# Kernel tuning notes

Measured on AMD Instinct MI355X. Metric: run time of the kernel, lower is better.

The kernel has to match this reference:

```python
import jax, jax.numpy as jnp
import numpy as np

B, T, C = 2, 2048, 1024
H, D, R = 16, 64, 32  # heads, head_dim, compression rank (R < D)


def setup_inputs() -> dict:
    key = jax.random.key(0)
    ks = jax.random.split(key, 8)
    s = 0.02
    return {
        "hidden_states": jax.random.normal(ks[0], (B, T, C), jnp.float32),
        "c_attn_w": jax.random.normal(ks[1], (C, 3 * C), jnp.float32) * s,
        "c_attn_b": jnp.zeros((3 * C,), jnp.float32),
        "c_proj_w": jax.random.normal(ks[2], (C, C), jnp.float32) * s,
        "c_proj_b": jnp.zeros((C,), jnp.float32),
        "wk_c": jax.random.normal(ks[3], (D, R), jnp.float32) * (1.0 / np.sqrt(D)),
        "wk_e": jax.random.normal(ks[4], (R, D), jnp.float32) * (1.0 / np.sqrt(R)),
        "wv_c": jax.random.normal(ks[5], (D, R), jnp.float32) * (1.0 / np.sqrt(D)),
        "wv_e": jax.random.normal(ks[6], (R, D), jnp.float32) * (1.0 / np.sqrt(R)),
    }


def reference(hidden_states, c_attn_w, c_attn_b, c_proj_w, c_proj_b,
              wk_c, wk_e, wv_c, wv_e):
    b, t, c = hidden_states.shape
    # GPT2 Conv1D: x @ W + b, then split into Q, K, V
    qkv = hidden_states @ c_attn_w + c_attn_b  # [B,T,3C]
    q, k, v = jnp.split(qkv, 3, axis=-1)

    def split_heads(x):  # [B,T,C] -> [B,H,T,D]
        return x.reshape(b, t, H, D).transpose(0, 2, 1, 3)

    q = split_heads(q)
    k = split_heads(k)
    v = split_heads(v)

    # Low-rank KV compression then expansion (rank R < D path)
    k_lat = jnp.einsum('bhtd,dr->bhtr', k, wk_c)  # [B,H,T,R]
    v_lat = jnp.einsum('bhtd,dr->bhtr', v, wv_c)
    k_exp = jnp.einsum('bhtr,rd->bhtd', k_lat, wk_e)  # [B,H,T,D]
    v_exp = jnp.einsum('bhtr,rd->bhtd', v_lat, wv_e)

    # Causal SDPA (attention_mask is None and q_len > 1 -> is_causal=True)
    scale = 1.0 / np.sqrt(D).astype(np.float32)
    scores = jnp.einsum('bhqd,bhkd->bhqk', q, k_exp) * scale  # [B,H,T,T]
    causal = jnp.tril(jnp.ones((t, t), dtype=bool))
    scores = jnp.where(causal[None, None], scores, jnp.finfo(scores.dtype).min)
    probs = jax.nn.softmax(scores, axis=-1)
    attn = jnp.einsum('bhqk,bhkd->bhqd', probs, v_exp)  # [B,H,T,D]

    # Merge heads and output projection
    attn = attn.transpose(0, 2, 1, 3).reshape(b, t, c)
    out = attn @ c_proj_w + c_proj_b
    return out
```

## Files before the change

kernel.cpp:

```cpp
#include <hip/hip_runtime.h>
#include <cstddef>

typedef __attribute__((ext_vector_type(8))) __bf16 bf16x8;
typedef __attribute__((ext_vector_type(4))) float f32x4;
typedef unsigned short u16;
typedef unsigned int   u32;

#define SCLF (0.125f * 1.44269504f)

__device__ __forceinline__ u16 f2bf(float f){
  union { float f; u32 u; } v; v.f = f;
  u32 r = v.u + 0x7FFFu + ((v.u >> 16) & 1u);
  return (u16)(r >> 16);
}
__device__ __forceinline__ u32 cvtpk(float lo, float hi){
  u32 r; asm("v_cvt_pk_bf16_f32 %0, %1, %2" : "=v"(r) : "v"(lo), "v"(hi)); return r;
}
__device__ __forceinline__ void gll16(const void* g, void* l){
  __builtin_amdgcn_global_load_lds((__attribute__((address_space(1))) void*)g,
                                   (__attribute__((address_space(3))) void*)l, 16, 0, 0);
}

__global__ __launch_bounds__(256) void prep_fused(const float* __restrict__ x,
      const float* __restrict__ Wa, const float* __restrict__ ba, const float* __restrict__ Wp,
      const float* __restrict__ kc, const float* __restrict__ ke,
      const float* __restrict__ vc, const float* __restrict__ ve,
      u16* __restrict__ Xb, float* __restrict__ b2,
      u16* __restrict__ Wt, u16* __restrict__ W2t){
  __shared__ __align__(16) char PS[28928];
  float* SH = (float*)PS;
  u16* As = (u16*)(PS + 16640);
  u16* Bs = (u16*)(PS + 16640 + 8192);
  const int bid = blockIdx.x, tid = threadIdx.x;

  if (bid < 4096){
    int i = bid*256 + tid;
    float4 v = ((const float4*)x)[i];
    uint2 r; r.x = cvtpk(v.x, v.y); r.y = cvtpk(v.z, v.w);
    ((uint2*)Xb)[i] = r;
    return;
  }
  if (bid < 4099){
    const int part = bid - 4096;
    float* BaL = SH;
    float* W65 = SH + 1024;
    *(float4*)&BaL[tid*4] = *(const float4*)&ba[part*1024 + tid*4];
    {
      const float* msrc = (part==0) ? ke : (part==1) ? kc : vc;
      #pragma unroll
      for (int i=0;i<8;++i){
        int idx = tid + i*256;
        float v = msrc[idx];
        int r, d;
        if (part == 0){ r = idx >> 6; d = idx & 63; }
        else          { d = idx >> 5; r = idx & 31; }
        W65[r*65 + d] = v;
      }
    }
    __syncthreads();
    const float scl = (part==0) ? SCLF : 1.f;
    #pragma unroll
    for (int t=0;t<2;++t){
      int l = tid + t*256;
      int hh = l >> 5, r = l & 31;
      float acc = 0.f;
      for (int d=0;d<64;++d) acc += BaL[hh*64 + d] * W65[r*65 + d];
      b2[part*512 + l] = acc * scl;
    }
    return;
  }

  const int wv = tid>>6, ln = tid&63;
  const int lr = ln&15, g8 = (ln>>4)*8, gq = ln>>4;
  const int swz = (lr&7)*8;

  if (bid < 4867){
    const int f = bid - 4099;
    const int cc = f & 15, ph = f >> 4;
    const int part = ph >> 4;
    const int c0 = cc*64;
    {
      int r = tid>>3, d8 = tid&7;
      float v[8];
      if (part == 0){
        #pragma unroll
        for (int j=0;j<8;++j) v[j] = ke[r*64 + d8*8 + j]*SCLF;
      } else {
        const float* m = (part==1) ? kc : vc;
        #pragma unroll
        for (int j=0;j<8;++j) v[j] = m[(d8*8+j)*32 + r];
      }
      uint4 w; w.x=cvtpk(v[0],v[1]); w.y=cvtpk(v[2],v[3]); w.z=cvtpk(v[4],v[5]); w.w=cvtpk(v[6],v[7]);
      *(uint4*)&Bs[r*64 + ((d8 ^ (r&7))*8)] = w;
    }
    #pragma unroll
    for (int p=0;p<2;++p){
      int g2 = p*256 + tid;
      int row = g2>>3, gcol = g2&7;
      const float* src = Wa + (size_t)(c0+row)*3072 + ph*64 + gcol*8;
      float4 a = ((const float4*)src)[0], b = ((const float4*)src)[1];
      uint4 w; w.x=cvtpk(a.x,a.y); w.y=cvtpk(a.z,a.w); w.z=cvtpk(b.x,b.y); w.w=cvtpk(b.z,b.w);
      *(uint4*)&As[row*64 + ((gcol ^ (row&7))*8)] = w;
    }
    __syncthreads();
    f32x4 acc[2] = {};
    const int wr = (wv>>1)*32, wn = wv&1;
    #pragma unroll
    for (int ks=0;ks<2;++ks){
      int off = (ks*32 + g8) ^ swz;
      bf16x8 bf = *(const bf16x8*)&Bs[(wn*16+lr)*64 + off];
      #pragma unroll
      for (int mt=0;mt<2;++mt){
        bf16x8 af = *(const bf16x8*)&As[(wr+mt*16+lr)*64 + off];
        acc[mt] = __builtin_amdgcn_mfma_f32_16x16x32_bf16(af, bf, acc[mt], 0,0,0);
      }
    }
    const int n = part*512 + (ph&15)*32 + wn*16 + lr;
    #pragma unroll
    for (int mt=0;mt<2;++mt){
      union { u16 s[4]; uint2 v; } pk;
      #pragma unroll
      for (int r=0;r<4;++r) pk.s[r] = f2bf(acc[mt][r]);
      *(uint2*)&Wt[(size_t)n*1024 + c0 + wr + mt*16 + 4*gq] = pk.v;
    }
  } else {
    const int f = bid - 4867;
    const int cc = f & 15, ph = f >> 4;
    const int c0 = cc*64;
    {
      int r = tid>>2, c4 = (tid&3)*16;
      const float* src = Wp + (size_t)(ph*64 + r)*1024 + c0 + c4;
      float4 v0 = ((const float4*)src)[0], v1 = ((const float4*)src)[1],
             v2 = ((const float4*)src)[2], v3 = ((const float4*)src)[3];
      float* dst = &SH[r*65 + c4];
      dst[0]=v0.x; dst[1]=v0.y; dst[2]=v0.z; dst[3]=v0.w;
      dst[4]=v1.x; dst[5]=v1.y; dst[6]=v1.z; dst[7]=v1.w;
      dst[8]=v2.x; dst[9]=v2.y; dst[10]=v2.z; dst[11]=v2.w;
      dst[12]=v3.x; dst[13]=v3.y; dst[14]=v3.z; dst[15]=v3.w;
    }
    {
      int r = tid>>3, d8 = tid&7;
      float v[8];
      #pragma unroll
      for (int j=0;j<8;++j) v[j] = ve[r*64 + d8*8 + j];
      uint4 w; w.x=cvtpk(v[0],v[1]); w.y=cvtpk(v[2],v[3]); w.z=cvtpk(v[4],v[5]); w.w=cvtpk(v[6],v[7]);
      *(uint4*)&Bs[r*64 + ((d8 ^ (r&7))*8)] = w;
    }
    __syncthreads();
    #pragma unroll
    for (int p=0;p<2;++p){
      int g2 = p*256 + tid;
      int j = g2>>3, d8 = g2&7;
      float v[8];
      #pragma unroll
      for (int jj=0;jj<8;++jj) v[jj] = SH[(d8*8+jj)*65 + j];
      uint4 w; w.x=cvtpk(v[0],v[1]); w.y=cvtpk(v[2],v[3]); w.z=cvtpk(v[4],v[5]); w.w=cvtpk(v[6],v[7]);
      *(uint4*)&As[j*64 + ((d8 ^ (j&7))*8)] = w;
    }
    __syncthreads();
    f32x4 acc[2] = {};
    const int wr = (wv>>1)*32, wn = wv&1;
    #pragma unroll
    for (int ks=0;ks<2;++ks){
      int off = (ks*32 + g8) ^ swz;
      bf16x8 bf = *(const bf16x8*)&Bs[(wn*16+lr)*64 + off];
      #pragma unroll
      for (int mt=0;mt<2;++mt){
        bf16x8 af = *(const bf16x8*)&As[(wr+mt*16+lr)*64 + off];
        acc[mt] = __builtin_amdgcn_mfma_f32_16x16x32_bf16(af, bf, acc[mt], 0,0,0);
      }
    }
    const int col = ph*32 + wn*16 + lr;
    #pragma unroll
    for (int mt=0;mt<2;++mt)
      #pragma unroll
      for (int r=0;r<4;++r)
        W2t[(size_t)(c0 + wr + mt*16 + 4*gq + r)*512 + col] = f2bf(acc[mt][r]);
  }
}

template<typename OT>
__global__ __launch_bounds__(256) void gemm64(const u16* __restrict__ A, const u16* __restrict__ Bt,
        const float* __restrict__ bias, OT* __restrict__ C, u16* __restrict__ Vt,
        int M, int N, int K, int ldc){
  __shared__ u16 Bs[128*64];
  const int nwg = gridDim.x * gridDim.y;
  const int id  = blockIdx.x + gridDim.x * blockIdx.y;
  const int nid = (id & 7) * (nwg >> 3) + (id >> 3);
  const int bx = nid % gridDim.x, by = nid / gridDim.x;
  const int tid = threadIdx.x, wv = tid>>6, ln = tid&63;
  const int lr = ln&15, g8 = (ln>>4)*8, gq = ln>>4;
  const int m0 = bx*64, n0 = by*128;
  const int wr = (wv>>1)*32, wc = (wv&1)*64;
  const int lrow = ln>>3, lcol = ((ln&7) ^ lrow)*8;
  const int swz = (lr&7)*8;
  const u16* aptr = A + (size_t)(m0 + wr + lr)*K + gq*8;
  f32x4 acc[2][4] = {};
  const int nk = K >> 6;
  for (int kt=0; kt<nk; ++kt){
    #pragma unroll
    for (int it=0; it<4; ++it){
      int bc = wv*4 + it;
      int row = bc*8 + lrow;
      gll16(Bt + (size_t)(n0+row)*K + kt*64 + lcol, &Bs[bc*512]);
    }
    bf16x8 aF[2][2];
    #pragma unroll
    for (int mt=0;mt<2;++mt)
      #pragma unroll
      for (int ks=0;ks<2;++ks)
        aF[mt][ks] = *(const bf16x8*)(aptr + (size_t)(mt*16)*K + kt*64 + ks*32);
    __syncthreads();
    #pragma unroll
    for (int ks=0; ks<2; ++ks){
      int off = (ks*32 + g8) ^ swz;
      bf16x8 bfr[4];
      #pragma unroll
      for (int nt=0;nt<4;++nt) bfr[nt] = *(const bf16x8*)&Bs[(wc+nt*16+lr)*64 + off];
      #pragma unroll
      for (int mt=0;mt<2;++mt)
        #pragma unroll
        for (int nt=0;nt<4;++nt)
          acc[mt][nt] = __builtin_amdgcn_mfma_f32_16x16x32_bf16(aF[mt][ks], bfr[nt], acc[mt][nt], 0,0,0);
    }
    __syncthreads();
  }
  if (Vt && n0 >= 1024){
    #pragma unroll
    for (int mt=0;mt<2;++mt){
      int row0 = m0 + wr + mt*16 + 4*(ln>>4);
      int tin  = row0 & 2047;
      int p0 = 4*((tin>>4)&1) + 8*((tin>>2)&3) + 32*(tin>>5);
      size_t vbase = (size_t)(row0 >> 11) * 512;
      #pragma unroll
      for (int nt=0;nt<4;++nt){
        int col = n0 + wc + nt*16 + lr;
        float bv = bias[col];
        int nlat = col - 1024;
        union { u16 s[4]; uint2 v; } pk;
        #pragma unroll
        for (int r=0;r<4;++r) pk.s[r] = f2bf(acc[mt][nt][r] + bv);
        *(uint2*)&Vt[(vbase + nlat)*2048 + p0] = pk.v;
      }
    }
  } else {
    #pragma unroll
    for (int mt=0;mt<2;++mt){
      int row = m0 + wr + mt*16 + 4*(ln>>4);
      #pragma unroll
      for (int nt=0;nt<4;++nt){
        int col = n0 + wc + nt*16 + lr;
        float bv = bias[col];
        #pragma unroll
        for (int r=0;r<4;++r){
          float v = acc[mt][nt][r] + bv;
          if constexpr (sizeof(OT) == 2) C[(size_t)(row+r)*ldc + col] = f2bf(v);
          else                           C[(size_t)(row+r)*ldc + col] = v;
        }
      }
    }
  }
}

__global__ __launch_bounds__(256, 4) void attn_fwd(const u16* __restrict__ QKV,
            const u16* __restrict__ Vt, u16* __restrict__ Out){
  const int bh = blockIdx.x;
  const int y = blockIdx.y;
  const int qt = (y < 8) ? y : (y < 16) ? 23 - y : (y < 24) ? y : 55 - y;
  const int b = bh >> 4, h = bh & 15;
  const int tid = threadIdx.x, wv = tid>>6, ln = tid&63;
  const int sg = wv>>1, wvL = wv&1;
  const int lr = ln&15, gq = ln>>4;
  __shared__ __align__(16) char SMEM[32768];
  u16* KB0 = (u16*)SMEM           + (sg*2    )*2048;
  u16* KB1 = (u16*)SMEM           + (sg*2 + 1)*2048;
  u16* VB0 = (u16*)(SMEM + 16384) + (sg*2    )*2048;
  u16* VB1 = (u16*)(SMEM + 16384) + (sg*2 + 1)*2048;
  const int q0 = qt*64;
  const size_t base = (size_t)(b*2048) * 1536;
  const u16* qrowA = QKV + base + (size_t)(q0 + wvL*32 + lr)*1536 + h*32;
  bf16x8 qfA = *(const bf16x8*)(qrowA + gq*8);
  bf16x8 qfB = *(const bf16x8*)(qrowA + (size_t)16*1536 + gq*8);
  const int qgA = q0 + wvL*32 + lr, qgB = qgA + 16;
  f32x4 oA0 = {}, oA1 = {}, oB0 = {}, oB1 = {};
  float lA = 0.f, lB = 0.f;
  const u16* ksrc = QKV + base + 512 + h*32;
  const u16* vsrc = Vt + (size_t)(bh*32)*2048;

  const int ci = wvL*64 + ln;
  const int rK = ci>>2, cK = 8*((ci&3) ^ (rK&3));
  const int rV = ci>>3, cV = 8*((ci&7) ^ (rV&7));

  int offK[4], offV[2][2];
  #pragma unroll
  for (int nt=0;nt<4;++nt)
    offK[nt] = (nt*16+lr)*64 + ((gq*16) ^ ((lr&3)<<4));
  #pragma unroll
  for (int dt=0;dt<2;++dt)
    #pragma unroll
    for (int c=0;c<2;++c)
      offV[dt][c] = (dt*16+lr)*128 + ((c*64 + gq*16) ^ ((lr&7)<<4));

  if (sg <= qt){
    gll16(ksrc + (size_t)(sg*64 + rK)*1536 + cK,      KB0 + wvL*512);
    gll16(ksrc + (size_t)(sg*64 + 32 + rK)*1536 + cK, KB0 + 1024 + wvL*512);
    gll16(vsrc + (size_t)rV*2048 + sg*64 + cV,        VB0 + wvL*512);
    gll16(vsrc + (size_t)(16+rV)*2048 + sg*64 + cV,   VB0 + 1024 + wvL*512);
  }
  __syncthreads();
  const u16* kpa = ksrc + (size_t)(sg*64 + 128 + rK)*1536 + cK;
  const u16* kpb = ksrc + (size_t)(sg*64 + 160 + rK)*1536 + cK;
  const u16* vpa = vsrc + (size_t)rV*2048 + sg*64 + 128 + cV;
  const u16* vpb = vsrc + (size_t)(16+rV)*2048 + sg*64 + 128 + cV;
  const size_t KSTEP = (size_t)128*1536;

  #define ABODY(II, KBC, VBC, KBN, VBN) do { \
    const int kt = 2*(II) + sg; \
    if (kt + 2 <= qt){ \
      gll16(kpa, (KBN) + wvL*512); \
      gll16(kpb, (KBN) + 1024 + wvL*512); \
      gll16(vpa, (VBN) + wvL*512); \
      gll16(vpb, (VBN) + 1024 + wvL*512); \
      kpa += KSTEP; kpb += KSTEP; vpa += 128; vpb += 128; \
    } \
    if (kt <= qt){ \
      f32x4 sA[4] = {}, sB[4] = {}; \
      __builtin_amdgcn_s_setprio(1); \
      _Pragma("unroll") for (int nt=0;nt<4;++nt){ \
        bf16x8 k0 = *(const bf16x8*)((const char*)(KBC) + offK[nt]); \
        sA[nt] = __builtin_amdgcn_mfma_f32_16x16x32_bf16(k0, qfA, sA[nt], 0,0,0); \
        sB[nt] = __builtin_amdgcn_mfma_f32_16x16x32_bf16(k0, qfB, sB[nt], 0,0,0); \
      } \
      __builtin_amdgcn_s_setprio(0); \
      if (kt == qt){ \
        const int kv0 = kt*64; \
        _Pragma("unroll") for (int nt=0;nt<4;++nt) \
        _Pragma("unroll") for (int r=0;r<4;++r){ \
          int k = kv0 + nt*16 + 4*gq + r; \
          if (k > qgA) sA[nt][r] = -1e30f; \
          if (k > qgB) sB[nt][r] = -1e30f; \
        } \
      } \
      union { u32 u[4]; bf16x8 v; } paA0, paA1, paB0, paB1; \
      { \
        float p0,p1,p2,p3,p4,p5,p6,p7; \
        p0=__builtin_amdgcn_exp2f(sA[0][0]); p1=__builtin_amdgcn_exp2f(sA[0][1]); \
        p2=__builtin_amdgcn_exp2f(sA[0][2]); p3=__builtin_amdgcn_exp2f(sA[0][3]); \
        p4=__builtin_amdgcn_exp2f(sA[1][0]); p5=__builtin_amdgcn_exp2f(sA[1][1]); \
        p6=__builtin_amdgcn_exp2f(sA[1][2]); p7=__builtin_amdgcn_exp2f(sA[1][3]); \
        lA += ((p0+p1)+(p2+p3)) + ((p4+p5)+(p6+p7)); \
        paA0.u[0]=cvtpk(p0,p1); paA0.u[1]=cvtpk(p2,p3); paA0.u[2]=cvtpk(p4,p5); paA0.u[3]=cvtpk(p6,p7); \
        p0=__builtin_amdgcn_exp2f(sA[2][0]); p1=__builtin_amdgcn_exp2f(sA[2][1]); \
        p2=__builtin_amdgcn_exp2f(sA[2][2]); p3=__builtin_amdgcn_exp2f(sA[2][3]); \
        p4=__builtin_amdgcn_exp2f(sA[3][0]); p5=__builtin_amdgcn_exp2f(sA[3][1]); \
        p6=__builtin_amdgcn_exp2f(sA[3][2]); p7=__builtin_amdgcn_exp2f(sA[3][3]); \
        lA += ((p0+p1)+(p2+p3)) + ((p4+p5)+(p6+p7)); \
        paA1.u[0]=cvtpk(p0,p1); paA1.u[1]=cvtpk(p2,p3); paA1.u[2]=cvtpk(p4,p5); paA1.u[3]=cvtpk(p6,p7); \
        p0=__builtin_amdgcn_exp2f(sB[0][0]); p1=__builtin_amdgcn_exp2f(sB[0][1]); \
        p2=__builtin_amdgcn_exp2f(sB[0][2]); p3=__builtin_amdgcn_exp2f(sB[0][3]); \
        p4=__builtin_amdgcn_exp2f(sB[1][0]); p5=__builtin_amdgcn_exp2f(sB[1][1]); \
        p6=__builtin_amdgcn_exp2f(sB[1][2]); p7=__builtin_amdgcn_exp2f(sB[1][3]); \
        lB += ((p0+p1)+(p2+p3)) + ((p4+p5)+(p6+p7)); \
        paB0.u[0]=cvtpk(p0,p1); paB0.u[1]=cvtpk(p2,p3); paB0.u[2]=cvtpk(p4,p5); paB0.u[3]=cvtpk(p6,p7); \
        p0=__builtin_amdgcn_exp2f(sB[2][0]); p1=__builtin_amdgcn_exp2f(sB[2][1]); \
        p2=__builtin_amdgcn_exp2f(sB[2][2]); p3=__builtin_amdgcn_exp2f(sB[2][3]); \
        p4=__builtin_amdgcn_exp2f(sB[3][0]); p5=__builtin_amdgcn_exp2f(sB[3][1]); \
        p6=__builtin_amdgcn_exp2f(sB[3][2]); p7=__builtin_amdgcn_exp2f(sB[3][3]); \
        lB += ((p0+p1)+(p2+p3)) + ((p4+p5)+(p6+p7)); \
        paB1.u[0]=cvtpk(p0,p1); paB1.u[1]=cvtpk(p2,p3); paB1.u[2]=cvtpk(p4,p5); paB1.u[3]=cvtpk(p6,p7); \
      } \
      __builtin_amdgcn_s_setprio(1); \
      { \
        bf16x8 v00 = *(const bf16x8*)((const char*)(VBC) + offV[0][0]); \
        bf16x8 v10 = *(const bf16x8*)((const char*)(VBC) + offV[1][0]); \
        bf16x8 v01 = *(const bf16x8*)((const char*)(VBC) + offV[0][1]); \
        bf16x8 v11 = *(const bf16x8*)((const char*)(VBC) + offV[1][1]); \
        oA0 = __builtin_amdgcn_mfma_f32_16x16x32_bf16(paA0.v, v00, oA0, 0,0,0); \
        oA1 = __builtin_amdgcn_mfma_f32_16x16x32_bf16(paA0.v, v10, oA1, 0,0,0); \
        oB0 = __builtin_amdgcn_mfma_f32_16x16x32_bf16(paB0.v, v00, oB0, 0,0,0); \
        oB1 = __builtin_amdgcn_mfma_f32_16x16x32_bf16(paB0.v, v10, oB1, 0,0,0); \
        oA0 = __builtin_amdgcn_mfma_f32_16x16x32_bf16(paA1.v, v01, oA0, 0,0,0); \
        oA1 = __builtin_amdgcn_mfma_f32_16x16x32_bf16(paA1.v, v11, oA1, 0,0,0); \
        oB0 = __builtin_amdgcn_mfma_f32_16x16x32_bf16(paB1.v, v01, oB0, 0,0,0); \
        oB1 = __builtin_amdgcn_mfma_f32_16x16x32_bf16(paB1.v, v11, oB1, 0,0,0); \
      } \
      __builtin_amdgcn_s_setprio(0); \
    } \
    __syncthreads(); \
  } while(0)

  const int nmax = (qt + 2) >> 1;
  const int jmax = (nmax + 1) >> 1;
  for (int j = 0; j < jmax; ++j){
    ABODY(2*j,   KB0, VB0, KB1, VB1);
    ABODY(2*j+1, KB1, VB1, KB0, VB0);
  }
  lA += __shfl_xor(lA, 16); lA += __shfl_xor(lA, 32);
  lB += __shfl_xor(lB, 16); lB += __shfl_xor(lB, 32);

  float* MO = (float*)SMEM;
  float* ML = (float*)(SMEM + 12288);
  if (sg == 1){
    #pragma unroll
    for (int r=0;r<4;++r){
      int rowA = wvL*32 + 4*gq + r;
      MO[rowA*34 + lr]            = oA0[r];
      MO[rowA*34 + 16 + lr]       = oA1[r];
      MO[(rowA+16)*34 + lr]       = oB0[r];
      MO[(rowA+16)*34 + 16 + lr]  = oB1[r];
    }
    if (gq == 0){ ML[wvL*32 + lr] = lA; ML[wvL*32 + 16 + lr] = lB; }
  }
  __syncthreads();
  if (sg == 0){
    float lSA = lA + ML[wvL*32 + lr];
    float lSB = lB + ML[wvL*32 + 16 + lr];
    float lA_o[4], lB_o[4];
    #pragma unroll
    for (int r=0;r<4;++r){ lA_o[r] = __shfl(lSA, 4*gq + r); lB_o[r] = __shfl(lSB, 4*gq + r); }
    #pragma unroll
    for (int r=0;r<4;++r){
      int rowA = wvL*32 + 4*gq + r;
      float vA0 = (oA0[r] + MO[rowA*34 + lr])           / lA_o[r];
      float vA1 = (oA1[r] + MO[rowA*34 + 16 + lr])      / lA_o[r];
      float vB0 = (oB0[r] + MO[(rowA+16)*34 + lr])      / lB_o[r];
      float vB1 = (oB1[r] + MO[(rowA+16)*34 + 16 + lr]) / lB_o[r];
      size_t obA = (size_t)(b*2048 + q0 + rowA)*512 + h*32;
      Out[obA + lr]      = f2bf(vA0);
      Out[obA + 16 + lr] = f2bf(vA1);
      size_t obB = obA + (size_t)16*512;
      Out[obB + lr]      = f2bf(vB0);
      Out[obB + 16 + lr] = f2bf(vB1);
    }
  }
}

#define WS_B2   0u
#define WS_WT   8192u
#define WS_W2T  (WS_WT + 3145728u)
#define WS_XB   (WS_W2T + 1048576u)
#define WS_QKV  (WS_XB + 8388608u)
#define WS_VT   (WS_QKV + 12582912u)
#define WS_ATT  (WS_VT + 4194304u)

extern "C" void kernel_launch(void* const* d_in, const int* in_sizes, int n_in,
                              void* d_out, int out_size, void* d_ws, size_t ws_size,
                              hipStream_t stream) {
  const float* x  = (const float*)d_in[0];
  const float* Wa = (const float*)d_in[1];
  const float* ba = (const float*)d_in[2];
  const float* Wp = (const float*)d_in[3];
  const float* bp = (const float*)d_in[4];
  const float* kc = (const float*)d_in[5];
  const float* ke = (const float*)d_in[6];
  const float* vc = (const float*)d_in[7];
  const float* ve = (const float*)d_in[8];
  float* out = (float*)d_out;
  char* ws = (char*)d_ws;
  float* b2  = (float*)(ws + WS_B2);
  u16* Wt    = (u16*)(ws + WS_WT);
  u16* W2t   = (u16*)(ws + WS_W2T);
  u16* Xb    = (u16*)(ws + WS_XB);
  u16* QKVb  = (u16*)(ws + WS_QKV);
  u16* Vt    = (u16*)(ws + WS_VT);
  u16* Att   = (u16*)(ws + WS_ATT);

  prep_fused<<<5123, 256, 0, stream>>>(x, Wa, ba, Wp, kc, ke, vc, ve, Xb, b2, Wt, W2t);
  gemm64<u16><<<dim3(64,12), 256, 0, stream>>>(Xb, Wt, b2, QKVb, Vt, 4096, 1536, 1024, 1536);
  attn_fwd<<<dim3(32,32), 256, 0, stream>>>(QKVb, Vt, Att);
  gemm64<float><<<dim3(64,8), 256, 0, stream>>>(Att, W2t, bp, out, (u16*)nullptr, 4096, 1024, 512, 1024);
}
```

Before: 83.01 us.

## Split prep kernel and stage GEMM A tiles through LDS via async loads

Splits the monolithic prep kernel into an x-conversion/bias kernel that handles four float4 elements per thread, and a separate weight-folding kernel launched on a 2D grid. In gemm64 the A operand now goes into LDS with global_load_lds, using the same swizzle as B, instead of being read directly from global memory into registers. This is meant to give coalesced A loads and fewer scattered global reads, at the cost of more LDS, one extra kernel launch, and LDS reads for the A fragments.

```diff
diff --git a/kernel.cpp b/kernel.cpp
--- a/kernel.cpp
+++ b/kernel.cpp
@@ -21,27 +21,23 @@
                                    (__attribute__((address_space(3))) void*)l, 16, 0, 0);
 }
 
-__global__ __launch_bounds__(256) void prep_fused(const float* __restrict__ x,
-      const float* __restrict__ Wa, const float* __restrict__ ba, const float* __restrict__ Wp,
-      const float* __restrict__ kc, const float* __restrict__ ke,
-      const float* __restrict__ vc, const float* __restrict__ ve,
-      u16* __restrict__ Xb, float* __restrict__ b2,
-      u16* __restrict__ Wt, u16* __restrict__ W2t){
-  __shared__ __align__(16) char PS[28928];
-  float* SH = (float*)PS;
-  u16* As = (u16*)(PS + 16640);
-  u16* Bs = (u16*)(PS + 16640 + 8192);
+__global__ __launch_bounds__(256) void prep_x(const float* __restrict__ x,
+      const float* __restrict__ ba, const float* __restrict__ kc,
+      const float* __restrict__ ke, const float* __restrict__ vc,
+      u16* __restrict__ Xb, float* __restrict__ b2){
+  __shared__ float SH[3104];
   const int bid = blockIdx.x, tid = threadIdx.x;
-
-  if (bid < 4096){
-    int i = bid*256 + tid;
-    float4 v = ((const float4*)x)[i];
-    uint2 r; r.x = cvtpk(v.x, v.y); r.y = cvtpk(v.z, v.w);
-    ((uint2*)Xb)[i] = r;
-    return;
-  }
-  if (bid < 4099){
-    const int part = bid - 4096;
+  if (bid < 1024){
+    int i0 = bid*1024 + tid;
+    #pragma unroll
+    for (int t=0;t<4;++t){
+      int i = i0 + t*256;
+      float4 v = ((const float4*)x)[i];
+      uint2 r; r.x = cvtpk(v.x, v.y); r.y = cvtpk(v.z, v.w);
+      ((uint2*)Xb)[i] = r;
+    }
+  } else {
+    const int part = bid - 1024;
     float* BaL = SH;
     float* W65 = SH + 1024;
     *(float4*)&BaL[tid*4] = *(const float4*)&ba[part*1024 + tid*4];
@@ -67,18 +63,27 @@
       for (int d=0;d<64;++d) acc += BaL[hh*64 + d] * W65[r*65 + d];
       b2[part*512 + l] = acc * scl;
     }
-    return;
-  }
-
+  }
+}
+
+__global__ __launch_bounds__(256) void fold_f32(const float* __restrict__ Wa,
+      const float* __restrict__ Wp, const float* __restrict__ kc,
+      const float* __restrict__ ke, const float* __restrict__ vc,
+      const float* __restrict__ ve, u16* __restrict__ Wt, u16* __restrict__ W2t){
+  __shared__ __align__(16) char PS[28928];
+  float* SH = (float*)PS;
+  u16* As = (u16*)(PS + 16640);
+  u16* Bs = (u16*)(PS + 16640 + 8192);
+  const int cc = blockIdx.x, y = blockIdx.y;
+  const int tid = threadIdx.x;
   const int wv = tid>>6, ln = tid&63;
   const int lr = ln&15, g8 = (ln>>4)*8, gq = ln>>4;
   const int swz = (lr&7)*8;
-
-  if (bid < 4867){
-    const int f = bid - 4099;
-    const int cc = f & 15, ph = f >> 4;
+  const int c0 = cc*64;
+
+  if (y < 48){
+    const int ph = y;
     const int part = ph >> 4;
-    const int c0 = cc*64;
     {
       int r = tid>>3, d8 = tid&7;
       float v[8];
@@ -124,9 +129,7 @@
       *(uint2*)&Wt[(size_t)n*1024 + c0 + wr + mt*16 + 4*gq] = pk.v;
     }
   } else {
-    const int f = bid - 4867;
-    const int cc = f & 15, ph = f >> 4;
-    const int c0 = cc*64;
+    const int ph = y - 48;
     {
       int r = tid>>2, c4 = (tid&3)*16;
       const float* src = Wp + (size_t)(ph*64 + r)*1024 + c0 + c4;
@@ -183,45 +186,47 @@
 __global__ __launch_bounds__(256) void gemm64(const u16* __restrict__ A, const u16* __restrict__ Bt,
         const float* __restrict__ bias, OT* __restrict__ C, u16* __restrict__ Vt,
         int M, int N, int K, int ldc){
+  __shared__ u16 As[64*64];
   __shared__ u16 Bs[128*64];
   const int nwg = gridDim.x * gridDim.y;
   const int id  = blockIdx.x + gridDim.x * blockIdx.y;
   const int nid = (id & 7) * (nwg >> 3) + (id >> 3);
   const int bx = nid % gridDim.x, by = nid / gridDim.x;
   const int tid = threadIdx.x, wv = tid>>6, ln = tid&63;
-  const int lr = ln&15, g8 = (ln>>4)*8, gq = ln>>4;
+  const int lr = ln&15, g8 = (ln>>4)*8;
   const int m0 = bx*64, n0 = by*128;
   const int wr = (wv>>1)*32, wc = (wv&1)*64;
   const int lrow = ln>>3, lcol = ((ln&7) ^ lrow)*8;
   const int swz = (lr&7)*8;
-  const u16* aptr = A + (size_t)(m0 + wr + lr)*K + gq*8;
   f32x4 acc[2][4] = {};
   const int nk = K >> 6;
   for (int kt=0; kt<nk; ++kt){
     #pragma unroll
-    for (int it=0; it<4; ++it){
-      int bc = wv*4 + it;
-      int row = bc*8 + lrow;
-      gll16(Bt + (size_t)(n0+row)*K + kt*64 + lcol, &Bs[bc*512]);
-    }
-    bf16x8 aF[2][2];
-    #pragma unroll
-    for (int mt=0;mt<2;++mt)
-      #pragma unroll
-      for (int ks=0;ks<2;++ks)
-        aF[mt][ks] = *(const bf16x8*)(aptr + (size_t)(mt*16)*K + kt*64 + ks*32);
+    for (int it=0; it<6; ++it){
+      int chunk = wv*6 + it;
+      if (chunk < 8){
+        int row = chunk*8 + lrow;
+        gll16(A + (size_t)(m0+row)*K + kt*64 + lcol, &As[chunk*512]);
+      } else {
+        int bc = chunk - 8;
+        int row = bc*8 + lrow;
+        gll16(Bt + (size_t)(n0+row)*K + kt*64 + lcol, &Bs[bc*512]);
+      }
+    }
     __syncthreads();
     #pragma unroll
     for (int ks=0; ks<2; ++ks){
       int off = (ks*32 + g8) ^ swz;
-      bf16x8 bfr[4];
+      bf16x8 af[2], bfr[4];
+      #pragma unroll
+      for (int mt=0;mt<2;++mt) af[mt]  = *(const bf16x8*)&As[(wr+mt*16+lr)*64 + off];
       #pragma unroll
       for (int nt=0;nt<4;++nt) bfr[nt] = *(const bf16x8*)&Bs[(wc+nt*16+lr)*64 + off];
       #pragma unroll
       for (int mt=0;mt<2;++mt)
         #pragma unroll
         for (int nt=0;nt<4;++nt)
-          acc[mt][nt] = __builtin_amdgcn_mfma_f32_16x16x32_bf16(aF[mt][ks], bfr[nt], acc[mt][nt], 0,0,0);
+          acc[mt][nt] = __builtin_amdgcn_mfma_f32_16x16x32_bf16(af[mt], bfr[nt], acc[mt][nt], 0,0,0);
     }
     __syncthreads();
   }
@@ -465,7 +470,8 @@
   u16* Vt    = (u16*)(ws + WS_VT);
   u16* Att   = (u16*)(ws + WS_ATT);
 
-  prep_fused<<<5123, 256, 0, stream>>>(x, Wa, ba, Wp, kc, ke, vc, ve, Xb, b2, Wt, W2t);
+  prep_x<<<1027, 256, 0, stream>>>(x, ba, kc, ke, vc, Xb, b2);
+  fold_f32<<<dim3(16,64), 256, 0, stream>>>(Wa, Wp, kc, ke, vc, ve, Wt, W2t);
   gemm64<u16><<<dim3(64,12), 256, 0, stream>>>(Xb, Wt, b2, QKVb, Vt, 4096, 1536, 1024, 1536);
   attn_fwd<<<dim3(32,32), 256, 0, stream>>>(QKVb, Vt, Att);
   gemm64<float><<<dim3(64,8), 256, 0, stream>>>(Att, W2t, bp, out, (u16*)nullptr, 4096, 1024, 512, 1024);
```

After: 69.34 us. 1.2x faster.
